# Kernel tuning notes

Measured on AMD Instinct MI355X. Metric: run time of the kernel, lower is better.

The kernel has to match this reference:

```python
import jax, jax.numpy as jnp
import numpy as np


def setup_inputs() -> dict:
    key = jax.random.key(0)
    k1, k2 = jax.random.split(key)
    B, T, D, K = 8, 4096, 256, 1024
    z = jax.random.normal(k1, (B, T, D), dtype=jnp.float32)
    codebook = jax.random.uniform(k2, (K, D), dtype=jnp.float32)
    return {"z": z, "codebook": codebook}


def reference(z, codebook):
    # Squared L2 distance via dot-product decomposition (same argmin as
    # the broadcasted squared-difference in the original module, without
    # materializing the (B,T,K,D) intermediate).
    #   ||z - c||^2 = ||z||^2 - 2 z.c + ||c||^2
    z_sq = jnp.sum(z * z, axis=-1, keepdims=True)            # (B,T,1)
    c_sq = jnp.sum(codebook * codebook, axis=-1)             # (K,)
    cross = jnp.einsum("btd,kd->btk", z, codebook)           # (B,T,K)
    l2_distance = z_sq - 2.0 * cross + c_sq                  # (B,T,K)
    codebook_indices = jnp.argmin(l2_distance, axis=-1)      # (B,T)
    z_q = codebook[codebook_indices]                         # (B,T,D)
    # Straight-through estimator
    z_q = z + jax.lax.stop_gradient(z_q - z)
    return (z_q, codebook_indices)
```

## Files before the change

kernel.cpp:

```cpp
#include <hip/hip_runtime.h>
#include <math.h>

#define NTOK   32768
#define NDIM   256
#define NCODE  1024
#define CHUNK  4096

typedef _Float16 f16x8 __attribute__((ext_vector_type(8)));
typedef float    f32x4 __attribute__((ext_vector_type(4)));

__global__ __launch_bounds__(256) void prep_cb(
        const float* __restrict__ cb,
        _Float16* __restrict__ ch, _Float16* __restrict__ cl,
        float* __restrict__ csq) {
    const int L   = blockIdx.x * 256 + threadIdx.x;
    const int row = L >> 5;
    const int g   = L & 31;

    const float* src = cb + (size_t)row * NDIM + g * 8;
    float4 a0 = *(const float4*)src;
    float4 a1 = *(const float4*)(src + 4);
    float v[8] = {a0.x, a0.y, a0.z, a0.w, a1.x, a1.y, a1.z, a1.w};
    f16x8 hi, lo;
    float s = 0.f;
    #pragma unroll
    for (int e = 0; e < 8; ++e) {
        _Float16 h = (_Float16)v[e];
        hi[e] = h;
        lo[e] = (_Float16)(v[e] - (float)h);
        s += v[e] * v[e];
    }
    const int r = row & 127;
    const size_t dst = (size_t)((row >> 7) * 8 + (g >> 2)) * CHUNK
                     + (r >> 4) * 512 + (g & 3) * 128 + (r & 15) * 8;
    *(f16x8*)&ch[dst] = hi;
    *(f16x8*)&cl[dst] = lo;
    #pragma unroll
    for (int off = 16; off > 0; off >>= 1) s += __shfl_down(s, off, 32);
    if ((threadIdx.x & 31) == 0) csq[row] = s;
}


#define LOADP(c, npr, H, L) do {                                             \
    const _Float16* _bh = pbh + (size_t)(c) * 4096 + (npr) * 1024;           \
    const _Float16* _bl = pbl + (size_t)(c) * 4096 + (npr) * 1024;           \
    H[0] = *(const f16x8*)_bh;                                               \
    H[1] = *(const f16x8*)(_bh + 512);                                       \
    L[0] = *(const f16x8*)_bl;                                               \
    L[1] = *(const f16x8*)(_bl + 512);                                       \
} while (0)

#define STEP(ph, pr, CH, CL, NH, NL, NC, NPR, FIRSTZ, DOPREF) do {           \
    if (DOPREF) LOADP(NC, NPR, NH, NL);                                      \
    __builtin_amdgcn_s_setprio(1);                                           \
    _Pragma("unroll")                                                        \
    for (int _mt = 0; _mt < 2; ++_mt)                                        \
        _Pragma("unroll")                                                    \
        for (int _i = 0; _i < 2; ++_i) {                                     \
            const int _t = (pr) * 2 + _i;                                    \
            acc[_mt][_t] = __builtin_amdgcn_mfma_f32_16x16x32_f16(           \
                ah[_mt][(ph)], CH[_i],                                       \
                (FIRSTZ) ? zz : acc[_mt][_t], 0, 0, 0);                      \
            acc[_mt][_t] = __builtin_amdgcn_mfma_f32_16x16x32_f16(           \
                al[_mt][(ph)], CH[_i], acc[_mt][_t], 0, 0, 0);               \
            acc[_mt][_t] = __builtin_amdgcn_mfma_f32_16x16x32_f16(           \
                ah[_mt][(ph)], CL[_i], acc[_mt][_t], 0, 0, 0);               \
        }                                                                    \
    __builtin_amdgcn_s_setprio(0);                                           \
} while (0)

#define STRIP(s, LASTPREF) do {                                              \
    const int _gb = (s) * 8;                                                 \
    STEP(0, 0, PAh, PAl, PBh, PBl, _gb + 0, 1, 1, 1);                        \
    STEP(0, 1, PBh, PBl, PAh, PAl, _gb + 1, 0, 1, 1);                        \
    STEP(1, 0, PAh, PAl, PBh, PBl, _gb + 1, 1, 0, 1);                        \
    STEP(1, 1, PBh, PBl, PAh, PAl, _gb + 2, 0, 0, 1);                        \
    STEP(2, 0, PAh, PAl, PBh, PBl, _gb + 2, 1, 0, 1);                        \
    STEP(2, 1, PBh, PBl, PAh, PAl, _gb + 3, 0, 0, 1);                        \
    STEP(3, 0, PAh, PAl, PBh, PBl, _gb + 3, 1, 0, 1);                        \
    STEP(3, 1, PBh, PBl, PAh, PAl, _gb + 4, 0, 0, 1);                        \
    STEP(4, 0, PAh, PAl, PBh, PBl, _gb + 4, 1, 0, 1);                        \
    STEP(4, 1, PBh, PBl, PAh, PAl, _gb + 5, 0, 0, 1);                        \
    STEP(5, 0, PAh, PAl, PBh, PBl, _gb + 5, 1, 0, 1);                        \
    STEP(5, 1, PBh, PBl, PAh, PAl, _gb + 6, 0, 0, 1);                        \
    STEP(6, 0, PAh, PAl, PBh, PBl, _gb + 6, 1, 0, 1);                        \
    STEP(6, 1, PBh, PBl, PAh, PAl, _gb + 7, 0, 0, 1);                        \
    STEP(7, 0, PAh, PAl, PBh, PBl, _gb + 7, 1, 0, 1);                        \
    STEP(7, 1, PBh, PBl, PAh, PAl, _gb + 8, 0, 0, LASTPREF);                 \
} while (0)

#define FOLD(S) do {                                                         \
    float cs[4];                                                             \
    _Pragma("unroll")                                                        \
    for (int _t = 0; _t < 4; ++_t)                                           \
        cs[_t] = csq[(S) * 128 + (nx * 4 + _t) * 16 + lr];                   \
    _Pragma("unroll")                                                        \
    for (int _mt = 0; _mt < 2; ++_mt)                                        \
        _Pragma("unroll")                                                    \
        for (int _r = 0; _r < 4; ++_r)                                       \
            _Pragma("unroll")                                                \
            for (int _t = 0; _t < 4; ++_t) {                                 \
                float _v = cs[_t] - 2.0f * acc[_mt][_t][_r];                 \
                int   _n = (S) * 128 + (nx * 4 + _t) * 16 + lr;              \
                if (_v < bv[_mt][_r] ||                                      \
                    (_v == bv[_mt][_r] && _n < bi[_mt][_r])) {               \
                    bv[_mt][_r] = _v; bi[_mt][_r] = _n;                      \
                }                                                            \
            }                                                                \
} while (0)

__global__ __launch_bounds__(256, 2) void vq_main(
        const float* __restrict__ z,
        const _Float16* __restrict__ ch, const _Float16* __restrict__ cl,
        const float* __restrict__ csq, const float* __restrict__ cb,
        float* __restrict__ zq, float* __restrict__ io) {
    __shared__ float sval[128];
    __shared__ int   sidx[128];
    __shared__ int   bestS[64];

    const int tid  = threadIdx.x;
    const int w    = tid >> 6;
    const int lane = tid & 63;
    const int quad = lane >> 4, lr = lane & 15;
    const int my   = w >> 1, nx = w & 1;
    const int m0   = blockIdx.x * 64;

    f16x8 ah[2][8], al[2][8];
    #pragma unroll
    for (int mt = 0; mt < 2; ++mt) {
        const float* zp = z + (size_t)(m0 + my * 32 + mt * 16 + lr) * NDIM
                        + quad * 8;
        #pragma unroll
        for (int c = 0; c < 8; ++c) {
            float4 a0 = *(const float4*)(zp + c * 32);
            float4 a1 = *(const float4*)(zp + c * 32 + 4);
            float v[8] = {a0.x, a0.y, a0.z, a0.w, a1.x, a1.y, a1.z, a1.w};
            #pragma unroll
            for (int e = 0; e < 8; ++e) {
                _Float16 h = (_Float16)v[e];
                ah[mt][c][e] = h;
                al[mt][c][e] = (_Float16)(v[e] - (float)h);
            }
        }
    }

    const _Float16* pbh = ch + nx * 2048 + quad * 128 + lr * 8;
    const _Float16* pbl = cl + nx * 2048 + quad * 128 + lr * 8;

    float bv[2][4];
    int   bi[2][4];
    #pragma unroll
    for (int mt = 0; mt < 2; ++mt)
        #pragma unroll
        for (int r = 0; r < 4; ++r) { bv[mt][r] = INFINITY; bi[mt][r] = 0x7fffffff; }

    const f32x4 zz = (f32x4){0.f, 0.f, 0.f, 0.f};
    f32x4 acc[2][4];

    f16x8 PAh[2], PAl[2], PBh[2], PBl[2];
    LOADP(0, 0, PAh, PAl);

    for (int s = 0; s < 7; ++s) {
        STRIP(s, 1);
        FOLD(s);
    }
    STRIP(7, 0);
    FOLD(7);

    #pragma unroll
    for (int msk = 1; msk < 16; msk <<= 1)
        #pragma unroll
        for (int mt = 0; mt < 2; ++mt)
            #pragma unroll
            for (int r = 0; r < 4; ++r) {
                float ov = __shfl_xor(bv[mt][r], msk, 64);
                int   oi = __shfl_xor(bi[mt][r], msk, 64);
                if (ov < bv[mt][r] || (ov == bv[mt][r] && oi < bi[mt][r])) {
                    bv[mt][r] = ov; bi[mt][r] = oi;
                }
            }

    if (lr == 0) {
        #pragma unroll
        for (int mt = 0; mt < 2; ++mt)
            #pragma unroll
            for (int r = 0; r < 4; ++r) {
                int row = my * 32 + mt * 16 + quad * 4 + r;
                sval[row * 2 + nx] = bv[mt][r];
                sidx[row * 2 + nx] = bi[mt][r];
            }
    }
    __syncthreads();

    if (tid < 64) {
        float v0 = sval[tid * 2], v1 = sval[tid * 2 + 1];
        int   i0 = sidx[tid * 2], i1 = sidx[tid * 2 + 1];
        bool take1 = (v1 < v0) || (v1 == v0 && i1 < i0);
        int best = take1 ? i1 : i0;
        bestS[tid] = best;
        io[m0 + tid] = (float)best;
    }
    __syncthreads();

    const int tr = tid >> 4, tc = tid & 15;
    #pragma unroll
    for (int p = 0; p < 4; ++p) {
        int row = p * 16 + tr;
        const float* src = cb + (size_t)bestS[row] * NDIM;
        float*       dst = zq + (size_t)(m0 + row) * NDIM;
        #pragma unroll
        for (int q = 0; q < 4; ++q) {
            int col = q * 64 + tc * 4;
            *(float4*)&dst[col] = *(const float4*)&src[col];
        }
    }
}

extern "C" void kernel_launch(void* const* d_in, const int* in_sizes, int n_in,
                              void* d_out, int out_size, void* d_ws, size_t ws_size,
                              hipStream_t stream) {
    const float* z  = (const float*)d_in[0];
    const float* cb = (const float*)d_in[1];

    float* zq = (float*)d_out;
    float* io = (float*)d_out + (size_t)NTOK * NDIM;

    _Float16* ch  = (_Float16*)d_ws;
    _Float16* cl  = ch + (size_t)NCODE * NDIM;
    float*    csq = (float*)(cl + (size_t)NCODE * NDIM);

    prep_cb<<<NCODE * 32 / 256, 256, 0, stream>>>(cb, ch, cl, csq);

    vq_main<<<NTOK / 64, 256, 0, stream>>>(z, ch, cl, csq, cb, zq, io);
}
```

Before: 133.2 us.

## Split work across 8 waves with one 16-row tile each, drop manual prefetch

```diff
diff --git a/kernel.cpp b/kernel.cpp
--- a/kernel.cpp
+++ b/kernel.cpp
@@ -40,76 +40,9 @@
     if ((threadIdx.x & 31) == 0) csq[row] = s;
 }
 
-
-#define LOADP(c, npr, H, L) do {                                             \
-    const _Float16* _bh = pbh + (size_t)(c) * 4096 + (npr) * 1024;           \
-    const _Float16* _bl = pbl + (size_t)(c) * 4096 + (npr) * 1024;           \
-    H[0] = *(const f16x8*)_bh;                                               \
-    H[1] = *(const f16x8*)(_bh + 512);                                       \
-    L[0] = *(const f16x8*)_bl;                                               \
-    L[1] = *(const f16x8*)(_bl + 512);                                       \
-} while (0)
-
-#define STEP(ph, pr, CH, CL, NH, NL, NC, NPR, FIRSTZ, DOPREF) do {           \
-    if (DOPREF) LOADP(NC, NPR, NH, NL);                                      \
-    __builtin_amdgcn_s_setprio(1);                                           \
-    _Pragma("unroll")                                                        \
-    for (int _mt = 0; _mt < 2; ++_mt)                                        \
-        _Pragma("unroll")                                                    \
-        for (int _i = 0; _i < 2; ++_i) {                                     \
-            const int _t = (pr) * 2 + _i;                                    \
-            acc[_mt][_t] = __builtin_amdgcn_mfma_f32_16x16x32_f16(           \
-                ah[_mt][(ph)], CH[_i],                                       \
-                (FIRSTZ) ? zz : acc[_mt][_t], 0, 0, 0);                      \
-            acc[_mt][_t] = __builtin_amdgcn_mfma_f32_16x16x32_f16(           \
-                al[_mt][(ph)], CH[_i], acc[_mt][_t], 0, 0, 0);               \
-            acc[_mt][_t] = __builtin_amdgcn_mfma_f32_16x16x32_f16(           \
-                ah[_mt][(ph)], CL[_i], acc[_mt][_t], 0, 0, 0);               \
-        }                                                                    \
-    __builtin_amdgcn_s_setprio(0);                                           \
-} while (0)
-
-#define STRIP(s, LASTPREF) do {                                              \
-    const int _gb = (s) * 8;                                                 \
-    STEP(0, 0, PAh, PAl, PBh, PBl, _gb + 0, 1, 1, 1);                        \
-    STEP(0, 1, PBh, PBl, PAh, PAl, _gb + 1, 0, 1, 1);                        \
-    STEP(1, 0, PAh, PAl, PBh, PBl, _gb + 1, 1, 0, 1);                        \
-    STEP(1, 1, PBh, PBl, PAh, PAl, _gb + 2, 0, 0, 1);                        \
-    STEP(2, 0, PAh, PAl, PBh, PBl, _gb + 2, 1, 0, 1);                        \
-    STEP(2, 1, PBh, PBl, PAh, PAl, _gb + 3, 0, 0, 1);                        \
-    STEP(3, 0, PAh, PAl, PBh, PBl, _gb + 3, 1, 0, 1);                        \
-    STEP(3, 1, PBh, PBl, PAh, PAl, _gb + 4, 0, 0, 1);                        \
-    STEP(4, 0, PAh, PAl, PBh, PBl, _gb + 4, 1, 0, 1);                        \
-    STEP(4, 1, PBh, PBl, PAh, PAl, _gb + 5, 0, 0, 1);                        \
-    STEP(5, 0, PAh, PAl, PBh, PBl, _gb + 5, 1, 0, 1);                        \
-    STEP(5, 1, PBh, PBl, PAh, PAl, _gb + 6, 0, 0, 1);                        \
-    STEP(6, 0, PAh, PAl, PBh, PBl, _gb + 6, 1, 0, 1);                        \
-    STEP(6, 1, PBh, PBl, PAh, PAl, _gb + 7, 0, 0, 1);                        \
-    STEP(7, 0, PAh, PAl, PBh, PBl, _gb + 7, 1, 0, 1);                        \
-    STEP(7, 1, PBh, PBl, PAh, PAl, _gb + 8, 0, 0, LASTPREF);                 \
-} while (0)
-
-#define FOLD(S) do {                                                         \
-    float cs[4];                                                             \
-    _Pragma("unroll")                                                        \
-    for (int _t = 0; _t < 4; ++_t)                                           \
-        cs[_t] = csq[(S) * 128 + (nx * 4 + _t) * 16 + lr];                   \
-    _Pragma("unroll")                                                        \
-    for (int _mt = 0; _mt < 2; ++_mt)                                        \
-        _Pragma("unroll")                                                    \
-        for (int _r = 0; _r < 4; ++_r)                                       \
-            _Pragma("unroll")                                                \
-            for (int _t = 0; _t < 4; ++_t) {                                 \
-                float _v = cs[_t] - 2.0f * acc[_mt][_t][_r];                 \
-                int   _n = (S) * 128 + (nx * 4 + _t) * 16 + lr;              \
-                if (_v < bv[_mt][_r] ||                                      \
-                    (_v == bv[_mt][_r] && _n < bi[_mt][_r])) {               \
-                    bv[_mt][_r] = _v; bi[_mt][_r] = _n;                      \
-                }                                                            \
-            }                                                                \
-} while (0)
-
-__global__ __launch_bounds__(256, 2) void vq_main(
+__global__ __launch_bounds__(512)
+__attribute__((amdgpu_waves_per_eu(4, 4)))
+void vq_main(
         const float* __restrict__ z,
         const _Float16* __restrict__ ch, const _Float16* __restrict__ cl,
         const float* __restrict__ csq, const float* __restrict__ cb,
@@ -122,14 +55,13 @@
     const int w    = tid >> 6;
     const int lane = tid & 63;
     const int quad = lane >> 4, lr = lane & 15;
-    const int my   = w >> 1, nx = w & 1;
+    const int rg   = w >> 1;
+    const int nx   = w & 1;
     const int m0   = blockIdx.x * 64;
 
-    f16x8 ah[2][8], al[2][8];
-    #pragma unroll
-    for (int mt = 0; mt < 2; ++mt) {
-        const float* zp = z + (size_t)(m0 + my * 32 + mt * 16 + lr) * NDIM
-                        + quad * 8;
+    f16x8 ah[8], al[8];
+    {
+        const float* zp = z + (size_t)(m0 + rg * 16 + lr) * NDIM + quad * 8;
         #pragma unroll
         for (int c = 0; c < 8; ++c) {
             float4 a0 = *(const float4*)(zp + c * 32);
@@ -138,8 +70,8 @@
             #pragma unroll
             for (int e = 0; e < 8; ++e) {
                 _Float16 h = (_Float16)v[e];
-                ah[mt][c][e] = h;
-                al[mt][c][e] = (_Float16)(v[e] - (float)h);
+                ah[c][e] = h;
+                al[c][e] = (_Float16)(v[e] - (float)h);
             }
         }
     }
@@ -147,48 +79,82 @@
     const _Float16* pbh = ch + nx * 2048 + quad * 128 + lr * 8;
     const _Float16* pbl = cl + nx * 2048 + quad * 128 + lr * 8;
 
-    float bv[2][4];
-    int   bi[2][4];
+    float bv[4];
+    int   bi[4];
     #pragma unroll
-    for (int mt = 0; mt < 2; ++mt)
-        #pragma unroll
-        for (int r = 0; r < 4; ++r) { bv[mt][r] = INFINITY; bi[mt][r] = 0x7fffffff; }
+    for (int r = 0; r < 4; ++r) { bv[r] = INFINITY; bi[r] = 0x7fffffff; }
 
     const f32x4 zz = (f32x4){0.f, 0.f, 0.f, 0.f};
-    f32x4 acc[2][4];
 
-    f16x8 PAh[2], PAl[2], PBh[2], PBl[2];
-    LOADP(0, 0, PAh, PAl);
+    for (int s = 0; s < 8; ++s) {
+        f32x4 acc0 = zz, acc1 = zz, acc2 = zz, acc3 = zz;
 
-    for (int s = 0; s < 7; ++s) {
-        STRIP(s, 1);
-        FOLD(s);
+        #pragma unroll
+        for (int c = 0; c < 8; ++c) {
+            const _Float16* ph = pbh + (size_t)(s * 8 + c) * CHUNK;
+            const _Float16* pl = pbl + (size_t)(s * 8 + c) * CHUNK;
+            f16x8 bh0 = *(const f16x8*)&ph[0];
+            f16x8 bh1 = *(const f16x8*)&ph[512];
+            f16x8 bl0 = *(const f16x8*)&pl[0];
+            f16x8 bl1 = *(const f16x8*)&pl[512];
+            __builtin_amdgcn_s_setprio(1);
+            acc0 = __builtin_amdgcn_mfma_f32_16x16x32_f16(ah[c], bh0, acc0, 0, 0, 0);
+            acc0 = __builtin_amdgcn_mfma_f32_16x16x32_f16(al[c], bh0, acc0, 0, 0, 0);
+            acc0 = __builtin_amdgcn_mfma_f32_16x16x32_f16(ah[c], bl0, acc0, 0, 0, 0);
+            acc1 = __builtin_amdgcn_mfma_f32_16x16x32_f16(ah[c], bh1, acc1, 0, 0, 0);
+            acc1 = __builtin_amdgcn_mfma_f32_16x16x32_f16(al[c], bh1, acc1, 0, 0, 0);
+            acc1 = __builtin_amdgcn_mfma_f32_16x16x32_f16(ah[c], bl1, acc1, 0, 0, 0);
+            __builtin_amdgcn_s_setprio(0);
+            f16x8 bh2 = *(const f16x8*)&ph[1024];
+            f16x8 bh3 = *(const f16x8*)&ph[1536];
+            f16x8 bl2 = *(const f16x8*)&pl[1024];
+            f16x8 bl3 = *(const f16x8*)&pl[1536];
+            __builtin_amdgcn_s_setprio(1);
+            acc2 = __builtin_amdgcn_mfma_f32_16x16x32_f16(ah[c], bh2, acc2, 0, 0, 0);
+            acc2 = __builtin_amdgcn_mfma_f32_16x16x32_f16(al[c], bh2, acc2, 0, 0, 0);
+            acc2 = __builtin_amdgcn_mfma_f32_16x16x32_f16(ah[c], bl2, acc2, 0, 0, 0);
+            acc3 = __builtin_amdgcn_mfma_f32_16x16x32_f16(ah[c], bh3, acc3, 0, 0, 0);
+            acc3 = __builtin_amdgcn_mfma_f32_16x16x32_f16(al[c], bh3, acc3, 0, 0, 0);
+            acc3 = __builtin_amdgcn_mfma_f32_16x16x32_f16(ah[c], bl3, acc3, 0, 0, 0);
+            __builtin_amdgcn_s_setprio(0);
+        }
+
+        #define FOLD1(ACC, T) do {                                           \
+            const int   _n  = s * 128 + (nx * 4 + (T)) * 16 + lr;            \
+            const float _cs = csq[_n];                                       \
+            _Pragma("unroll")                                                \
+            for (int _r = 0; _r < 4; ++_r) {                                 \
+                float _v = _cs - 2.0f * ACC[_r];                             \
+                if (_v < bv[_r] || (_v == bv[_r] && _n < bi[_r])) {          \
+                    bv[_r] = _v; bi[_r] = _n;                                \
+                }                                                            \
+            }                                                                \
+        } while (0)
+        FOLD1(acc0, 0);
+        FOLD1(acc1, 1);
+        FOLD1(acc2, 2);
+        FOLD1(acc3, 3);
+        #undef FOLD1
     }
-    STRIP(7, 0);
-    FOLD(7);
 
     #pragma unroll
     for (int msk = 1; msk < 16; msk <<= 1)
         #pragma unroll
-        for (int mt = 0; mt < 2; ++mt)
-            #pragma unroll
-            for (int r = 0; r < 4; ++r) {
-                float ov = __shfl_xor(bv[mt][r], msk, 64);
-                int   oi = __shfl_xor(bi[mt][r], msk, 64);
-                if (ov < bv[mt][r] || (ov == bv[mt][r] && oi < bi[mt][r])) {
-                    bv[mt][r] = ov; bi[mt][r] = oi;
-                }
+        for (int r = 0; r < 4; ++r) {
+            float ov = __shfl_xor(bv[r], msk, 64);
+            int   oi = __shfl_xor(bi[r], msk, 64);
+            if (ov < bv[r] || (ov == bv[r] && oi < bi[r])) {
+                bv[r] = ov; bi[r] = oi;
             }
+        }
 
     if (lr == 0) {
         #pragma unroll
-        for (int mt = 0; mt < 2; ++mt)
-            #pragma unroll
-            for (int r = 0; r < 4; ++r) {
-                int row = my * 32 + mt * 16 + quad * 4 + r;
-                sval[row * 2 + nx] = bv[mt][r];
-                sidx[row * 2 + nx] = bi[mt][r];
-            }
+        for (int r = 0; r < 4; ++r) {
+            int row = rg * 16 + quad * 4 + r;
+            sval[row * 2 + nx] = bv[r];
+            sidx[row * 2 + nx] = bi[r];
+        }
     }
     __syncthreads();
 
@@ -202,17 +168,13 @@
     }
     __syncthreads();
 
-    const int tr = tid >> 4, tc = tid & 15;
+    const int gr = tid >> 3, gc = tid & 7;
+    const float* src = cb + (size_t)bestS[gr] * NDIM;
+    float*       dst = zq + (size_t)(m0 + gr) * NDIM;
     #pragma unroll
-    for (int p = 0; p < 4; ++p) {
-        int row = p * 16 + tr;
-        const float* src = cb + (size_t)bestS[row] * NDIM;
-        float*       dst = zq + (size_t)(m0 + row) * NDIM;
-        #pragma unroll
-        for (int q = 0; q < 4; ++q) {
-            int col = q * 64 + tc * 4;
-            *(float4*)&dst[col] = *(const float4*)&src[col];
-        }
+    for (int q = 0; q < 8; ++q) {
+        int col = q * 32 + gc * 4;
+        *(float4*)&dst[col] = *(const float4*)&src[col];
     }
 }
 
@@ -231,5 +193,5 @@
 
     prep_cb<<<NCODE * 32 / 256, 256, 0, stream>>>(cb, ch, cl, csq);
 
-    vq_main<<<NTOK / 64, 256, 0, stream>>>(z, ch, cl, csq, cb, zq, io);
+    vq_main<<<NTOK / 64, 512, 0, stream>>>(z, ch, cl, csq, cb, zq, io);
 }
```

Measured after the change: 155.8 us. 1.17x slower.
